# Kernel tuning notes

Measured on AMD Instinct MI355X. Metric: run time of the kernel, lower is better.

The kernel has to match this reference:

```python
import jax, jax.numpy as jnp
import numpy as np

BS, SEQ, IN, H, L = 32, 2048, 512, 256, 2


def _cell(x_t, h, W1, b1, W2, b2):
    # blending1(x, x, x): gate1*x + (1-gate1)*x  (kept literal for faithfulness)
    g1 = jax.nn.sigmoid(x_t @ W1.T + b1)
    left = g1 * x_t + (1.0 - g1) * x_t
    # blending2(h, x, x): gate from x, blend h and x
    g2 = jax.nn.sigmoid(x_t @ W2.T + b2)
    right = g2 * h + (1.0 - g2) * x_t
    return jnp.tanh(left * right)


def _run_dir(x_seq, h0, W1, b1, W2, b2):
    # x_seq: [seq, bs, H]; sequential recurrence via scan
    def step(h, x_t):
        h_new = _cell(x_t, h, W1, b1, W2, b2)
        return h_new, h_new
    h_last, ys = jax.lax.scan(step, h0, x_seq)
    return ys, h_last  # ys: [seq, bs, H], h_last: [bs, H]


def setup_inputs() -> dict:
    key = jax.random.key(0)
    ks = jax.random.split(key, 7)
    std = 1.0 / np.sqrt(H)
    return {
        "x": jax.random.normal(ks[0], (BS, SEQ, IN), dtype=jnp.float32),
        "W_fc": jax.random.uniform(ks[1], (H, IN), jnp.float32, -std, std),
        "b_fc": jax.random.uniform(ks[2], (H,), jnp.float32, -std, std),
        "W1": jax.random.uniform(ks[3], (L, H, H), jnp.float32, -std, std),
        "b1": jax.random.uniform(ks[4], (L, H), jnp.float32, -std, std),
        "W2": jax.random.uniform(ks[5], (L, H, H), jnp.float32, -std, std),
        "b2": jax.random.uniform(ks[6], (L, H), jnp.float32, -std, std),
    }


def reference(x, W_fc, b_fc, W1, b1, W2, b2):
    bs, seq, _ = x.shape
    Hh = W_fc.shape[0]
    n_layers = W1.shape[0]
    # input projection, then duplicate along features: [bs, seq, 2H]
    h = x @ W_fc.T + b_fc
    xx = jnp.concatenate([h, h], axis=2)
    h_finals = []
    for i in range(n_layers):
        # split halves: left-to-right on first half, right-to-left on flipped second half
        ltr = jnp.swapaxes(xx[:, :, :Hh], 0, 1)                      # [seq, bs, H]
        rtl = jnp.swapaxes(jnp.flip(xx[:, :, Hh:], axis=1), 0, 1)    # [seq, bs, H]
        h0 = jnp.zeros((bs, Hh), dtype=xx.dtype)
        y_l, h_l = _run_dir(ltr, h0, W1[i], b1[i], W2[i], b2[i])
        y_r, h_r = _run_dir(rtl, h0, W1[i], b1[i], W2[i], b2[i])
        y_l = jnp.swapaxes(y_l, 0, 1)                                # [bs, seq, H]
        y_r = jnp.flip(jnp.swapaxes(y_r, 0, 1), axis=1)
        xx = jnp.concatenate([y_l, y_r], axis=2)                     # [bs, seq, 2H]
        h_finals.append(jnp.stack([h_l, h_r], axis=0))               # [2, bs, H]
    h_out = jnp.concatenate(h_finals, axis=0)                        # [2L, bs, H]
    return xx, h_out
```

## Files before the change

kernel.cpp:

```cpp
#include <hip/hip_runtime.h>

#define SEQL 2048
#define BSZ  32
#define HDIM 256
#define MTOT (BSZ*SEQL)
#define XXN  ((size_t)MTOT*512)

typedef short v8s __attribute__((ext_vector_type(8)));
typedef float v4f __attribute__((ext_vector_type(4)));
typedef const __attribute__((address_space(1))) void* gptr_t;
typedef __attribute__((address_space(3))) void* sptr_t;

__device__ __forceinline__ short f2bf(float f) {
  return __builtin_bit_cast(short, (__bf16)f);
}

__device__ __forceinline__ void gload16(const float* g, float* l) {
  __builtin_amdgcn_global_load_lds((gptr_t)g, (sptr_t)l, 16, 0, 0);
}

__global__ __launch_bounds__(256) void gemm_bias_act(
    const float* __restrict__ A, int sa,
    const float* __restrict__ W, int K,
    const float* __restrict__ bias,
    float* __restrict__ C, int act)
{
  __shared__ float lds[20480];

  int tid  = threadIdx.x;
  int nwg = (int)gridDim.x;
  int cpx = nwg >> 3;
  int bid = (int)blockIdx.x;
  int v   = (bid & 7) * cpx + (bid >> 3);
  int m0  = (v >> 1) * 128;
  int n0  = (v & 1) * 128;

  int lane = tid & 63;
  int w    = tid >> 6;
  int wr   = w >> 1, wc = w & 1;
  int quad = lane >> 4, r16 = lane & 15;

  int lrow = lane >> 3;
  int js   = (lane & 7) ^ lrow;
  const float* aSrc = A + (long)(m0 + w*8 + lrow)*sa + js*4;
  const float* wSrc = W + (long)(n0 + w*8 + lrow)*K  + js*4;

  auto stageA = [&](int buf, int kk) {
    const float* a = aSrc + kk;
    float* la = lds + buf*4096 + w*256;
    #pragma unroll
    for (int i = 0; i < 4; ++i) gload16(a + (long)i*32*sa, la + i*1024);
  };
  auto stageB = [&](int buf, int kk) {
    const float* b = wSrc + kk;
    float* lb = lds + 12288 + buf*4096 + w*256;
    #pragma unroll
    for (int i = 0; i < 4; ++i) gload16(b + (long)i*32*K, lb + i*1024);
  };

  int aoff[4][2], boff[4][2];
  #pragma unroll
  for (int i = 0; i < 4; ++i) {
    int ra_ = wr*64 + i*16 + r16, sA = ra_ & 7;
    aoff[i][0] = ra_*32 + ((2*quad)     ^ sA)*4;
    aoff[i][1] = ra_*32 + ((2*quad + 1) ^ sA)*4;
    int rb_ = wc*64 + i*16 + r16, sB = rb_ & 7;
    boff[i][0] = rb_*32 + ((2*quad)     ^ sB)*4;
    boff[i][1] = rb_*32 + ((2*quad + 1) ^ sB)*4;
  }

  auto loadfrag = [&](const float* base, const int* o) {
    float4 f0 = *(const float4*)(base + o[0]);
    float4 f1 = *(const float4*)(base + o[1]);
    v8s r;
    r[0] = f2bf(f0.x); r[1] = f2bf(f0.y); r[2] = f2bf(f0.z); r[3] = f2bf(f0.w);
    r[4] = f2bf(f1.x); r[5] = f2bf(f1.y); r[6] = f2bf(f1.z); r[7] = f2bf(f1.w);
    return r;
  };

  v4f acc[4][4];
  #pragma unroll
  for (int i = 0; i < 4; ++i)
    #pragma unroll
    for (int j = 0; j < 4; ++j)
      acc[i][j] = (v4f){0.f, 0.f, 0.f, 0.f};

  auto compute = [&](const float* Ab, const float* Bb) {
    v8s af[4], bfv[4];
    #pragma unroll
    for (int i = 0; i < 4; ++i) af[i]  = loadfrag(Ab, aoff[i]);
    #pragma unroll
    for (int j = 0; j < 4; ++j) bfv[j] = loadfrag(Bb, boff[j]);
    #pragma unroll
    for (int i = 0; i < 4; ++i)
      #pragma unroll
      for (int j = 0; j < 4; ++j)
        acc[i][j] = __builtin_amdgcn_mfma_f32_16x16x32_bf16(af[i], bfv[j], acc[i][j], 0, 0, 0);
  };

  stageB(0, 0);
  asm volatile("" ::: "memory");
  stageA(0, 0);
  asm volatile("" ::: "memory");
  stageA(1, 32);

  int nt = K >> 5;
  int ra = 0;
  for (int t = 0; t < nt - 1; ++t) {
    asm volatile("s_waitcnt vmcnt(4) lgkmcnt(0)" ::: "memory");
    __builtin_amdgcn_s_barrier();
    asm volatile("" ::: "memory");

    stageB((t + 1) & 1, (t + 1) * 32);
    asm volatile("" ::: "memory");
    if (t + 2 < nt) {
      int wb = ra + 2; if (wb >= 3) wb -= 3;
      stageA(wb, (t + 2) * 32);
    }

    compute(lds + ra*4096, lds + 12288 + (t & 1)*4096);
    ra = (ra == 2) ? 0 : ra + 1;
  }
  asm volatile("s_waitcnt vmcnt(0) lgkmcnt(0)" ::: "memory");
  __builtin_amdgcn_s_barrier();
  asm volatile("" ::: "memory");
  compute(lds + ra*4096, lds + 12288 + ((nt - 1) & 1)*4096);

  #pragma unroll
  for (int j = 0; j < 4; ++j) {
    int col = n0 + wc*64 + j*16 + r16;
    float bv = bias[col];
    #pragma unroll
    for (int i = 0; i < 4; ++i) {
      int rowb = m0 + wr*64 + i*16 + quad*4;
      #pragma unroll
      for (int r = 0; r < 4; ++r) {
        float vv = acc[i][j][r] + bv;
        if (act) {
          float e = __builtin_amdgcn_exp2f(vv * -1.4426950408889634f);
          vv = __builtin_amdgcn_rcpf(1.f + e);
        }
        C[(long)(rowb + r)*HDIM + col] = vv;
      }
    }
  }
}

__global__ __launch_bounds__(64) void recur(
    const float* __restrict__ X, int sx, int xoffR,
    const float* __restrict__ G, int sg, int goffR,
    float* __restrict__ Y, float* __restrict__ hout)
{
  const int T = 16;
  const int SEGS = 8;
  const int SEGLEN = SEQL / SEGS;
  const int WARM = 64;

  int blk = blockIdx.x & 255;
  int seg = blockIdx.x >> 8;
  int fg = blk & 3;
  int b  = (blk >> 2) & 31;
  int d  = blk >> 7;
  int f  = fg*64 + threadIdx.x;

  int u0    = seg*SEGLEN - (seg ? WARM : 0);
  int warmc = seg ? (WARM/T) : 0;
  int nc    = warmc + SEGLEN/T;
  int half  = nc >> 1;

  int stp  = d ? -1 : 1;
  int t0   = d ? (SEQL-1 - u0) : u0;
  int xoff = d ? xoffR : 0;
  int goff = d ? goffR : 0;

  const float* xc = X + (long)(b*SEQL + t0)*sx + xoff + f;
  const float* gc = G + (long)(b*SEQL + t0)*sg + goff + f;
  long xstep = (long)stp * sx;
  long gstep = (long)stp * sg;

  int ty0 = d ? (SEQL-1 - seg*SEGLEN) : seg*SEGLEN;
  float* yp = Y + (long)(b*SEQL + ty0)*512 + d*HDIM + f;
  long ystep = (long)stp * 512;

  const float K   = 2.8853900817779268f;
  const float mK2 = -5.7707801635558537f;

  float Ax[T], Ag[T], Bx[T], Bg[T], hb[T];
  #pragma unroll
  for (int j = 0; j < T; ++j) { Ax[j] = xc[xstep*j]; Ag[j] = gc[gstep*j]; }

  float r = 0.5f;

  auto compute = [&](float* xb, float* gb) {
    #pragma unroll
    for (int j = 0; j < T; ++j) {
      float x = xb[j], g = gb[j];
      float a = x * g;
      float m = a * mK2;
      float n = K * fmaf(x, x - a, a);
      float q = fmaf(m, r, n);
      float E = __builtin_amdgcn_exp2f(q);
      r = __builtin_amdgcn_rcpf(E + 1.0f);
      hb[j] = fmaf(-2.0f, r, 1.0f);
    }
  };
  auto flush = [&](int c) {
    if (c >= warmc) {
      #pragma unroll
      for (int j = 0; j < T; ++j) yp[ystep*j] = hb[j];
      yp += ystep*T;
    }
  };

  int c = 0;
  for (int it = 0; it < half; ++it) {
    const float* xn = xc + xstep*T;
    const float* gn = gc + gstep*T;
    #pragma unroll
    for (int j = 0; j < T; ++j) { Bx[j] = xn[xstep*j]; Bg[j] = gn[gstep*j]; }
    compute(Ax, Ag); flush(c);
    bool hv = (c+2 < nc);
    const float* xn2 = hv ? xn + xstep*T : xn;
    const float* gn2 = hv ? gn + gstep*T : gn;
    #pragma unroll
    for (int j = 0; j < T; ++j) { Ax[j] = xn2[xstep*j]; Ag[j] = gn2[gstep*j]; }
    compute(Bx, Bg); flush(c+1);
    xc = xn2; gc = gn2; c += 2;
  }

  if (seg == SEGS-1)
    hout[(size_t)d*BSZ*HDIM + (size_t)b*HDIM + f] = fmaf(-2.0f, r, 1.0f);
}

extern "C" void kernel_launch(void* const* d_in, const int* in_sizes, int n_in,
                              void* d_out, int out_size, void* d_ws, size_t ws_size,
                              hipStream_t stream) {
  const float* x    = (const float*)d_in[0];
  const float* W_fc = (const float*)d_in[1];
  const float* b_fc = (const float*)d_in[2];
  const float* W2   = (const float*)d_in[5];
  const float* b2   = (const float*)d_in[6];

  float* out  = (float*)d_out;
  float* bufA = (float*)d_ws;
  float* bufB = bufA + (size_t)MTOT*HDIM;
  float* xx   = out;
  float* hout = out + XXN;

  gemm_bias_act<<<1024, 256, 0, stream>>>(x, 512, W_fc, 512, b_fc, bufA, 0);
  gemm_bias_act<<<1024, 256, 0, stream>>>(bufA, HDIM, W2, HDIM, b2, bufB, 1);
  recur<<<2048, 64, 0, stream>>>(bufA, HDIM, 0, bufB, HDIM, 0, xx, hout);
  gemm_bias_act<<<2048, 256, 0, stream>>>(xx, HDIM, W2 + HDIM*HDIM, HDIM, b2 + HDIM, bufA, 1);
  recur<<<2048, 64, 0, stream>>>(xx, 512, 256, bufA, 512, 256, xx, hout + 2*BSZ*HDIM);
}
```

Before: 472.4 us.

## Fuse input projection with layer-0 gate GEMM and pre-convert weights to bf16

Adds a small kernel that converts W_fc and W2 to bf16 once per call. It merges the input-projection GEMM and the layer-0 gate GEMM into one 512-thread kernel: each block computes a full 128x256 tile of h, stores it to global memory and to LDS as bf16, then runs the second GEMM from LDS. The goal is to avoid re-reading h from global memory, save a launch, and halve weight traffic while removing per-fragment weight conversion. In exchange it uses a large shared-memory footprint, which limits occupancy, adds an extra launch, and needs workspace at a fixed offset.

```diff
diff --git a/kernel.cpp b/kernel.cpp
--- a/kernel.cpp
+++ b/kernel.cpp
@@ -18,58 +18,89 @@
 __device__ __forceinline__ void gload16(const float* g, float* l) {
   __builtin_amdgcn_global_load_lds((gptr_t)g, (sptr_t)l, 16, 0, 0);
 }
-
-__global__ __launch_bounds__(256) void gemm_bias_act(
-    const float* __restrict__ A, int sa,
-    const float* __restrict__ W, int K,
-    const float* __restrict__ bias,
-    float* __restrict__ C, int act)
+__device__ __forceinline__ void gload16s(const unsigned short* g, short* l) {
+  __builtin_amdgcn_global_load_lds((gptr_t)g, (sptr_t)l, 16, 0, 0);
+}
+
+__global__ __launch_bounds__(256) void wconv(
+    const float* __restrict__ Wfc, const float* __restrict__ W2,
+    unsigned short* __restrict__ out)
 {
-  __shared__ float lds[20480];
+  int i = blockIdx.x*256 + threadIdx.x;
+  int stride = 256 * gridDim.x;
+  for (int k = i; k < 131072; k += stride) {
+    out[k]          = (unsigned short)f2bf(Wfc[k]);
+    out[131072 + k] = (unsigned short)f2bf(W2[k]);
+  }
+}
+
+__global__ __launch_bounds__(512, 2) void gemm_fused12(
+    const float* __restrict__ A,
+    const unsigned short* __restrict__ Wfc,
+    const float* __restrict__ bfc,
+    const unsigned short* __restrict__ W2b,
+    const float* __restrict__ b2v,
+    float* __restrict__ Hglob,
+    float* __restrict__ G)
+{
+  __shared__ short smem[65536];
 
   int tid  = threadIdx.x;
-  int nwg = (int)gridDim.x;
-  int cpx = nwg >> 3;
-  int bid = (int)blockIdx.x;
-  int v   = (bid & 7) * cpx + (bid >> 3);
-  int m0  = (v >> 1) * 128;
-  int n0  = (v & 1) * 128;
+  int nwg  = (int)gridDim.x;
+  int cpx  = nwg >> 3;
+  int bid  = (int)blockIdx.x;
+  int v    = (bid & 7)*cpx + (bid >> 3);
+  int m0   = v * 128;
 
   int lane = tid & 63;
   int w    = tid >> 6;
-  int wr   = w >> 1, wc = w & 1;
+  int wr   = w >> 2, wc = w & 3;
   int quad = lane >> 4, r16 = lane & 15;
-
   int lrow = lane >> 3;
   int js   = (lane & 7) ^ lrow;
-  const float* aSrc = A + (long)(m0 + w*8 + lrow)*sa + js*4;
-  const float* wSrc = W + (long)(n0 + w*8 + lrow)*K  + js*4;
-
-  auto stageA = [&](int buf, int kk) {
+
+  const float* aSrc = A + (long)(m0 + w*16 + lrow)*512 + js*4;
+  int csB = (lane & 3) ^ ((lane >> 2) & 3);
+  const unsigned short* fcSrc = Wfc + (long)(w*32 + (lane >> 2))*512 + csB*8;
+  const unsigned short* w2Src = W2b + (long)(w*32 + (lane >> 2))*256 + csB*8;
+
+  float* Af  = (float*)smem;
+  short* Bf  = smem + 24576;
+  short* W2f = smem + 40960;
+
+  auto stageA1 = [&](int buf, int kk) {
     const float* a = aSrc + kk;
-    float* la = lds + buf*4096 + w*256;
-    #pragma unroll
-    for (int i = 0; i < 4; ++i) gload16(a + (long)i*32*sa, la + i*1024);
-  };
-  auto stageB = [&](int buf, int kk) {
-    const float* b = wSrc + kk;
-    float* lb = lds + 12288 + buf*4096 + w*256;
-    #pragma unroll
-    for (int i = 0; i < 4; ++i) gload16(b + (long)i*32*K, lb + i*1024);
-  };
-
-  int aoff[4][2], boff[4][2];
+    float* la = Af + buf*4096 + (w*2)*256;
+    gload16(a,          la);
+    gload16(a + 8*512,  la + 256);
+  };
+  auto stageB1 = [&](int buf, int kk) {
+    const unsigned short* g = fcSrc + kk;
+    short* lb = Bf + buf*8192 + (w*2)*512;
+    gload16s(g,           lb);
+    gload16s(g + 16*512,  lb + 512);
+  };
+  auto stageW2 = [&](int buf, int kk) {
+    const unsigned short* g = w2Src + kk;
+    short* lb = W2f + buf*8192 + (w*2)*512;
+    gload16s(g,           lb);
+    gload16s(g + 16*256,  lb + 512);
+  };
+
+  int aoff[4][2], boff[4];
   #pragma unroll
   for (int i = 0; i < 4; ++i) {
-    int ra_ = wr*64 + i*16 + r16, sA = ra_ & 7;
-    aoff[i][0] = ra_*32 + ((2*quad)     ^ sA)*4;
-    aoff[i][1] = ra_*32 + ((2*quad + 1) ^ sA)*4;
-    int rb_ = wc*64 + i*16 + r16, sB = rb_ & 7;
-    boff[i][0] = rb_*32 + ((2*quad)     ^ sB)*4;
-    boff[i][1] = rb_*32 + ((2*quad + 1) ^ sB)*4;
-  }
-
-  auto loadfrag = [&](const float* base, const int* o) {
+    int ra_ = wr*64 + i*16 + r16, s7 = r16 & 7;
+    aoff[i][0] = ra_*32 + ((2*quad)     ^ s7)*4;
+    aoff[i][1] = ra_*32 + ((2*quad + 1) ^ s7)*4;
+  }
+  #pragma unroll
+  for (int j = 0; j < 4; ++j) {
+    int n = wc*64 + j*16 + r16;
+    boff[j] = n*32 + ((quad ^ (r16 & 3))*8);
+  }
+
+  auto loadfragf = [&](const float* base, const int* o) {
     float4 f0 = *(const float4*)(base + o[0]);
     float4 f1 = *(const float4*)(base + o[1]);
     v8s r;
@@ -85,46 +116,219 @@
     for (int j = 0; j < 4; ++j)
       acc[i][j] = (v4f){0.f, 0.f, 0.f, 0.f};
 
-  auto compute = [&](const float* Ab, const float* Bb) {
-    v8s af[4], bfv[4];
-    #pragma unroll
-    for (int i = 0; i < 4; ++i) af[i]  = loadfrag(Ab, aoff[i]);
-    #pragma unroll
-    for (int j = 0; j < 4; ++j) bfv[j] = loadfrag(Bb, boff[j]);
+  auto compute1 = [&](int ab, int bb) {
+    const float* Ab = Af + ab*4096;
+    const short* Bb = Bf + bb*8192;
+    v8s af[4], bv[4];
+    #pragma unroll
+    for (int i = 0; i < 4; ++i) af[i] = loadfragf(Ab, aoff[i]);
+    #pragma unroll
+    for (int j = 0; j < 4; ++j) bv[j] = *(const v8s*)&Bb[boff[j]];
     #pragma unroll
     for (int i = 0; i < 4; ++i)
       #pragma unroll
       for (int j = 0; j < 4; ++j)
-        acc[i][j] = __builtin_amdgcn_mfma_f32_16x16x32_bf16(af[i], bfv[j], acc[i][j], 0, 0, 0);
-  };
-
-  stageB(0, 0);
+        acc[i][j] = __builtin_amdgcn_mfma_f32_16x16x32_bf16(af[i], bv[j], acc[i][j], 0, 0, 0);
+  };
+
+  stageW2(0, 0);  asm volatile("" ::: "memory");
+  stageW2(1, 32); asm volatile("" ::: "memory");
+  stageB1(0, 0);  asm volatile("" ::: "memory");
+  stageA1(0, 0);  asm volatile("" ::: "memory");
+  stageA1(1, 32);
+
+  int ra = 0;
+  for (int t = 0; t < 15; ++t) {
+    asm volatile("s_waitcnt vmcnt(2) lgkmcnt(0)" ::: "memory");
+    __builtin_amdgcn_s_barrier();
+    asm volatile("" ::: "memory");
+    stageB1((t + 1) & 1, (t + 1)*32);
+    asm volatile("" ::: "memory");
+    if (t + 2 < 16) { int wb = ra + 2; if (wb >= 3) wb -= 3; stageA1(wb, (t + 2)*32); }
+    compute1(ra, t & 1);
+    ra = (ra == 2) ? 0 : ra + 1;
+  }
+  asm volatile("s_waitcnt vmcnt(0) lgkmcnt(0)" ::: "memory");
+  __builtin_amdgcn_s_barrier();
   asm volatile("" ::: "memory");
-  stageA(0, 0);
+  compute1(ra, 1);
+
+  asm volatile("s_waitcnt lgkmcnt(0)" ::: "memory");
+  __builtin_amdgcn_s_barrier();
   asm volatile("" ::: "memory");
+
+  #pragma unroll
+  for (int j = 0; j < 4; ++j) {
+    int col = wc*64 + j*16 + r16;
+    float bv = bfc[col];
+    int colg = col >> 3, cl = col & 7;
+    #pragma unroll
+    for (int i = 0; i < 4; ++i) {
+      int rowl = wr*64 + i*16 + quad*4;
+      #pragma unroll
+      for (int r = 0; r < 4; ++r) {
+        int row = rowl + r;
+        float h = acc[i][j][r] + bv;
+        smem[row*256 + ((colg ^ (row & 7))*8) + cl] = f2bf(h);
+        Hglob[(long)(m0 + row)*HDIM + col] = h;
+      }
+    }
+  }
+
+  v4f acc2[4][4];
+  #pragma unroll
+  for (int i = 0; i < 4; ++i)
+    #pragma unroll
+    for (int j = 0; j < 4; ++j)
+      acc2[i][j] = (v4f){0.f, 0.f, 0.f, 0.f};
+
+  int rb = 0;
+  for (int s = 0; s < 8; ++s) {
+    asm volatile("s_waitcnt vmcnt(2) lgkmcnt(0)" ::: "memory");
+    __builtin_amdgcn_s_barrier();
+    asm volatile("" ::: "memory");
+    if (s + 2 < 8) { int wb = rb + 2; if (wb >= 3) wb -= 3; stageW2(wb, (s + 2)*32); }
+    const short* Wb = W2f + rb*8192;
+    v8s hf[4], wv[4];
+    #pragma unroll
+    for (int i = 0; i < 4; ++i) {
+      int m = wr*64 + i*16 + r16;
+      hf[i] = *(const v8s*)&smem[m*256 + (((s*4 + quad) ^ (r16 & 7))*8)];
+    }
+    #pragma unroll
+    for (int j = 0; j < 4; ++j) wv[j] = *(const v8s*)&Wb[boff[j]];
+    #pragma unroll
+    for (int i = 0; i < 4; ++i)
+      #pragma unroll
+      for (int j = 0; j < 4; ++j)
+        acc2[i][j] = __builtin_amdgcn_mfma_f32_16x16x32_bf16(hf[i], wv[j], acc2[i][j], 0, 0, 0);
+    rb = (rb == 2) ? 0 : rb + 1;
+  }
+
+  #pragma unroll
+  for (int j = 0; j < 4; ++j) {
+    int col = wc*64 + j*16 + r16;
+    float bv = b2v[col];
+    #pragma unroll
+    for (int i = 0; i < 4; ++i) {
+      int rowb = m0 + wr*64 + i*16 + quad*4;
+      #pragma unroll
+      for (int r = 0; r < 4; ++r) {
+        float vv = acc2[i][j][r] + bv;
+        float e = __builtin_amdgcn_exp2f(vv * -1.4426950408889634f);
+        vv = __builtin_amdgcn_rcpf(1.f + e);
+        G[(long)(rowb + r)*HDIM + col] = vv;
+      }
+    }
+  }
+}
+
+__global__ __launch_bounds__(256) void gemm_bias_act(
+    const float* __restrict__ A,
+    const unsigned short* __restrict__ W,
+    const float* __restrict__ bias,
+    float* __restrict__ C)
+{
+  __shared__ short smem3[32768];
+
+  int tid  = threadIdx.x;
+  int nwg  = (int)gridDim.x;
+  int cpx  = nwg >> 3;
+  int bid  = (int)blockIdx.x;
+  int v    = (bid & 7)*cpx + (bid >> 3);
+  int m0   = (v >> 1) * 128;
+  int n0   = (v & 1) * 128;
+
+  int lane = tid & 63;
+  int w    = tid >> 6;
+  int wr   = w >> 1, wc = w & 1;
+  int quad = lane >> 4, r16 = lane & 15;
+  int lrow = lane >> 3;
+  int js   = (lane & 7) ^ lrow;
+
+  const float* aSrc = A + (long)(m0 + w*8 + lrow)*HDIM + js*4;
+  int csB = (lane & 3) ^ ((lane >> 2) & 3);
+  const unsigned short* wSrc = W + (long)(n0 + w*32 + (lane >> 2))*HDIM + csB*8;
+
+  float* Af = (float*)smem3;
+  short* Bs = smem3 + 24576;
+
+  auto stageA = [&](int buf, int kk) {
+    const float* a = aSrc + kk;
+    float* la = Af + buf*4096 + w*256;
+    #pragma unroll
+    for (int i = 0; i < 4; ++i) gload16(a + (long)i*32*HDIM, la + i*1024);
+  };
+  auto stageB = [&](int buf, int kk) {
+    const unsigned short* g = wSrc + kk;
+    short* lb = Bs + buf*4096 + w*1024;
+    gload16s(g,           lb);
+    gload16s(g + 16*HDIM, lb + 512);
+  };
+
+  int aoff[4][2], boff[4];
+  #pragma unroll
+  for (int i = 0; i < 4; ++i) {
+    int ra_ = wr*64 + i*16 + r16, s7 = r16 & 7;
+    aoff[i][0] = ra_*32 + ((2*quad)     ^ s7)*4;
+    aoff[i][1] = ra_*32 + ((2*quad + 1) ^ s7)*4;
+  }
+  #pragma unroll
+  for (int j = 0; j < 4; ++j) {
+    int n = wc*64 + j*16 + r16;
+    boff[j] = n*32 + ((quad ^ (r16 & 3))*8);
+  }
+
+  auto loadfragf = [&](const float* base, const int* o) {
+    float4 f0 = *(const float4*)(base + o[0]);
+    float4 f1 = *(const float4*)(base + o[1]);
+    v8s r;
+    r[0] = f2bf(f0.x); r[1] = f2bf(f0.y); r[2] = f2bf(f0.z); r[3] = f2bf(f0.w);
+    r[4] = f2bf(f1.x); r[5] = f2bf(f1.y); r[6] = f2bf(f1.z); r[7] = f2bf(f1.w);
+    return r;
+  };
+
+  v4f acc[4][4];
+  #pragma unroll
+  for (int i = 0; i < 4; ++i)
+    #pragma unroll
+    for (int j = 0; j < 4; ++j)
+      acc[i][j] = (v4f){0.f, 0.f, 0.f, 0.f};
+
+  auto compute = [&](int ab, int bb) {
+    const float* Ab = Af + ab*4096;
+    const short* Bb = Bs + bb*4096;
+    v8s af[4], bv[4];
+    #pragma unroll
+    for (int i = 0; i < 4; ++i) af[i] = loadfragf(Ab, aoff[i]);
+    #pragma unroll
+    for (int j = 0; j < 4; ++j) bv[j] = *(const v8s*)&Bb[boff[j]];
+    #pragma unroll
+    for (int i = 0; i < 4; ++i)
+      #pragma unroll
+      for (int j = 0; j < 4; ++j)
+        acc[i][j] = __builtin_amdgcn_mfma_f32_16x16x32_bf16(af[i], bv[j], acc[i][j], 0, 0, 0);
+  };
+
+  stageB(0, 0);  asm volatile("" ::: "memory");
+  stageA(0, 0);  asm volatile("" ::: "memory");
   stageA(1, 32);
 
-  int nt = K >> 5;
   int ra = 0;
-  for (int t = 0; t < nt - 1; ++t) {
+  for (int t = 0; t < 7; ++t) {
     asm volatile("s_waitcnt vmcnt(4) lgkmcnt(0)" ::: "memory");
     __builtin_amdgcn_s_barrier();
     asm volatile("" ::: "memory");
-
-    stageB((t + 1) & 1, (t + 1) * 32);
+    stageB((t + 1) & 1, (t + 1)*32);
     asm volatile("" ::: "memory");
-    if (t + 2 < nt) {
-      int wb = ra + 2; if (wb >= 3) wb -= 3;
-      stageA(wb, (t + 2) * 32);
-    }
-
-    compute(lds + ra*4096, lds + 12288 + (t & 1)*4096);
+    if (t + 2 < 8) { int wb = ra + 2; if (wb >= 3) wb -= 3; stageA(wb, (t + 2)*32); }
+    compute(ra, t & 1);
     ra = (ra == 2) ? 0 : ra + 1;
   }
   asm volatile("s_waitcnt vmcnt(0) lgkmcnt(0)" ::: "memory");
   __builtin_amdgcn_s_barrier();
   asm volatile("" ::: "memory");
-  compute(lds + ra*4096, lds + 12288 + ((nt - 1) & 1)*4096);
+  compute(ra, 1);
 
   #pragma unroll
   for (int j = 0; j < 4; ++j) {
@@ -136,10 +340,8 @@
       #pragma unroll
       for (int r = 0; r < 4; ++r) {
         float vv = acc[i][j][r] + bv;
-        if (act) {
-          float e = __builtin_amdgcn_exp2f(vv * -1.4426950408889634f);
-          vv = __builtin_amdgcn_rcpf(1.f + e);
-        }
+        float e = __builtin_amdgcn_exp2f(vv * -1.4426950408889634f);
+        vv = __builtin_amdgcn_rcpf(1.f + e);
         C[(long)(rowb + r)*HDIM + col] = vv;
       }
     }
@@ -244,12 +446,13 @@
   float* out  = (float*)d_out;
   float* bufA = (float*)d_ws;
   float* bufB = bufA + (size_t)MTOT*HDIM;
+  unsigned short* wbf = (unsigned short*)(bufA + (size_t)50331648);
   float* xx   = out;
   float* hout = out + XXN;
 
-  gemm_bias_act<<<1024, 256, 0, stream>>>(x, 512, W_fc, 512, b_fc, bufA, 0);
-  gemm_bias_act<<<1024, 256, 0, stream>>>(bufA, HDIM, W2, HDIM, b2, bufB, 1);
+  wconv<<<128, 256, 0, stream>>>(W_fc, W2, wbf);
+  gemm_fused12<<<512, 512, 0, stream>>>(x, wbf, b_fc, wbf + 131072, b2, bufA, bufB);
   recur<<<2048, 64, 0, stream>>>(bufA, HDIM, 0, bufB, HDIM, 0, xx, hout);
-  gemm_bias_act<<<2048, 256, 0, stream>>>(xx, HDIM, W2 + HDIM*HDIM, HDIM, b2 + HDIM, bufA, 1);
+  gemm_bias_act<<<2048, 256, 0, stream>>>(xx, wbf + 196608, b2 + HDIM, bufA);
   recur<<<2048, 64, 0, stream>>>(xx, 512, 256, bufA, 512, 256, xx, hout + 2*BSZ*HDIM);
 }
```

After: 444.9 us. 5.8% less time.
